# Kernel tuning notes

Measured on AMD Instinct MI355X. Metric: run time of the kernel, lower is better.

## Reference

```python
import jax, jax.numpy as jnp
import numpy as np

_PROFILE = [2, 3, 4]  # direction exponents per scale -> 4, 8, 16 directions


def _make_filter_banks():
    """Build per-scale grouped-conv filter banks.
    Returns list of arrays [3*num_dirs, 1, k, k] (same filters tiled for R,G,B groups)."""
    banks = []
    for scale, exp in enumerate(_PROFILE):
        num_dirs = 2 ** exp
        size = 11 + 4 * scale
        center = size // 2
        coords = np.arange(size) - center
        X, Y = np.meshgrid(coords, coords)
        kernels = []
        for d in range(num_dirs):
            angle = np.pi * d / num_dirs
            Xr = X * np.cos(angle) + Y * np.sin(angle)
            Yr = -X * np.sin(angle) + Y * np.cos(angle)
            freq = 0.3 / 2 ** scale
            dir_bandwidth = 2.0
            env = np.exp(-(Xr ** 2 + (dir_bandwidth * Yr) ** 2) / (2 * (size / 4) ** 2))
            k = env * np.cos(2 * np.pi * freq * Xr)
            k = k / (np.abs(k).sum() + 1e-8)
            kernels.append(k)
        bank = np.stack(kernels)[:, None]          # [nd, 1, k, k]
        bank = np.tile(bank, (3, 1, 1, 1))          # [3*nd, 1, k, k] (groups = RGB)
        banks.append(jnp.asarray(bank, dtype=jnp.float32))
    return banks


def setup_inputs() -> dict:
    key = jax.random.key(0)
    rgb_image = jax.random.normal(key, (4, 3, 512, 512), dtype=jnp.float32)
    f0, f1, f2 = _make_filter_banks()
    return {"rgb_image": rgb_image, "f0": f0, "f1": f1, "f2": f2}


def _grouped_conv(x, w):
    # x: [B,3,H,W], w: [3*nd,1,k,k]; SAME padding (k odd), one group per RGB channel.
    p = w.shape[-1] // 2
    return jax.lax.conv_general_dilated(
        x, w, window_strides=(1, 1), padding=[(p, p), (p, p)],
        feature_group_count=3,
        dimension_numbers=("NCHW", "OIHW", "NCHW"))


def reference(rgb_image, f0, f1, f2):
    B, C, H, W = rgb_image.shape
    # Directional subbands per scale, grouped by channel: [B, 3, nd, H, W]
    s0 = _grouped_conv(rgb_image, f0).reshape(B, 3, 4, H, W)
    s1 = _grouped_conv(rgb_image, f1).reshape(B, 3, 8, H, W)
    s2 = _grouped_conv(rgb_image, f2).reshape(B, 3, 16, H, W)
    # Low-frequency branch: avg_pool2d(k=4,s=4) then bilinear upsample (align_corners=False)
    low = rgb_image.reshape(B, 3, H // 4, 4, W // 4, 4).mean(axis=(3, 5))
    low = jax.image.resize(low, (B, 3, H, W), method="linear")
    low = low[:, :, None]  # [B, 3, 1, H, W]
    # Per channel: [s0 dirs, s1 dirs, s2 dirs, low] -> 29 bands; 3 channels -> 87
    out = jnp.concatenate([s0, s1, s2, low], axis=2).reshape(B, 87, H, W)
    return out
```

## Files before the change

kernel.cpp:

```cpp
#include <hip/hip_runtime.h>
#include <hip/hip_bf16.h>

#define HW 512

typedef __attribute__((ext_vector_type(8))) short bf16x8;
typedef __attribute__((ext_vector_type(16))) float floatx16;

union BFrag { uint2 u2[2]; bf16x8 v; };

static __device__ inline ushort f2bf(float f) {
    __hip_bfloat16 h = __float2bfloat16(f);
    return *(ushort*)&h;
}

__device__ __align__(16) short g_afrag[(18 + 27 + 30) * 256 * 8];

template<int K, int NDIR, int SUB0, int OCTS, int NSTEP, int AOFF>
__device__ __forceinline__
void conv_body(ushort* __restrict__ s_img,
               const float* __restrict__ img, float* __restrict__ out,
               const int plane)
{
    constexpr int YPACK   = 32 / NDIR;
    constexpr int R       = K / 2;
    constexpr int TILE_W  = 128, TILE_H = 32;
    constexpr int NCHAIN  = TILE_H / YPACK;
    constexpr int CB      = 4;
    constexpr int NPASS   = NCHAIN / CB;
    constexpr int ROWS_A  = K + YPACK - 1;
    constexpr int EXT_Y   = (TILE_H - YPACK) + ROWS_A;
    constexpr int EXT_X   = 4 * 31 + 8 * (OCTS - 1) + 8;
    constexpr int SPX     = (EXT_X + 7) & ~7;
    constexpr int P       = (OCTS == 3) ? 3 : 1;
    constexpr int GSTRIDE = (2 * P / OCTS) * SPX;
    constexpr int NG      = NSTEP / P;
    static_assert(NSTEP % P == 0, "octet chunking must be exact");
    static_assert(NSTEP * 2 == ROWS_A * OCTS, "step count must cover octets");

    const int tid   = threadIdx.x;
    const int bx    = blockIdx.x, by = blockIdx.y;
    const int bb    = plane / 3, cc = plane % 3;
    const float* __restrict__ src = img + (size_t)plane * HW * HW;
    const int gx0 = bx * TILE_W, gy0 = by * TILE_H;

    constexpr int PAIRS = SPX / 2;
    for (int idx = tid; idx < EXT_Y * PAIRS; idx += 256) {
        const int row = idx / PAIRS;
        const int col = (idx - row * PAIRS) * 2;
        const int gy = gy0 - R + row;
        const int gx = gx0 - R + col;
        float v0 = 0.f, v1 = 0.f;
        if ((unsigned)gy < HW) {
            if ((unsigned)gx       < HW) v0 = src[gy * HW + gx];
            if ((unsigned)(gx + 1) < HW) v1 = src[gy * HW + gx + 1];
        }
        *(uint*)&s_img[row * SPX + col] = ((uint)f2bf(v1) << 16) | (uint)f2bf(v0);
    }
    __syncthreads();

    const int lane = tid & 63;
    const int r    = tid >> 6;
    const int n    = lane & 31;
    const int h    = lane >> 5;

    int base0[P];
    #pragma unroll
    for (int s0 = 0; s0 < P; ++s0) {
        const int c0   = 2 * s0 + h;
        const int dyu0 = c0 / OCTS, o0 = c0 - dyu0 * OCTS;
        base0[s0] = dyu0 * SPX + 8 * o0 + 4 * n;
    }

    const int px = gx0 + r + 4 * n;
    const short* __restrict__ abase = g_afrag + ((size_t)AOFF + tid) * 8;

    for (int p = 0; p < NPASS; ++p) {
        floatx16 acc[CB] = {};
        const ushort* bp = s_img + p * (CB * YPACK * SPX);
        const short*  ap = abase;
        for (int gi = 0; gi < NG; ++gi) {
            #pragma unroll
            for (int s0 = 0; s0 < P; ++s0) {
                const bf16x8 a = *(const bf16x8*)(ap + s0 * 256 * 8);
                #pragma unroll
                for (int i = 0; i < CB; ++i) {
                    const ushort* q = bp + (base0[s0] + i * (YPACK * SPX));
                    BFrag b;
                    b.u2[0] = *(const uint2*)q;
                    b.u2[1] = *(const uint2*)(q + 4);
                    acc[i] = __builtin_amdgcn_mfma_f32_32x32x16_bf16(a, b.v, acc[i], 0, 0, 0);
                }
            }
            bp += GSTRIDE;
            ap += P * 256 * 8;
        }
        #pragma unroll
        for (int i = 0; i < CB; ++i) {
            #pragma unroll
            for (int reg = 0; reg < 16; ++reg) {
                const int m  = (reg & 3) + 8 * (reg >> 2) + 4 * h;
                const int dd = m & (NDIR - 1);
                const int yo = m / NDIR;
                const int Y  = gy0 + (p * CB + i) * YPACK + yo;
                out[((size_t)(bb * 87 + cc * 29 + SUB0 + dd) * HW + Y) * HW + px] = acc[i][reg];
            }
        }
    }
}

#define SMEM_ELEMS 7600

__global__ __launch_bounds__(256, 4)
void fused_conv(const float* __restrict__ img, float* __restrict__ out)
{
    __shared__ __align__(16) ushort s_img[SMEM_ELEMS];
    const int z  = blockIdx.z;
    const int sc = z % 3;
    const int plane = z / 3;
    if (sc == 0) {
        conv_body<19, 16, 12, 3, 30, (18 + 27) * 256>(s_img, img, out, plane);
    } else if (sc == 1) {
        conv_body<15,  8,  4, 3, 27, 18 * 256>(s_img, img, out, plane);
    } else {
        conv_body<11,  4,  0, 2, 18, 0>(s_img, img, out, plane);
    }
}

template<int K, int NDIR, int OCTS, int NSTEP, int AOFF>
__device__ __forceinline__
void prep_body(const float* __restrict__ filt)
{
    const int tid  = threadIdx.x;
    const int lane = tid & 63, r = tid >> 6;
    const int m    = lane & 31, h = lane >> 5;
    const int dirm  = m & (NDIR - 1);
    const int yoffm = m / NDIR;
    for (int s = 0; s < NSTEP; ++s) {
        bf16x8 v;
        #pragma unroll
        for (int j = 0; j < 8; ++j) {
            const int c   = 2 * s + h;
            const int dyu = c / OCTS, o = c - dyu * OCTS;
            const int dy  = dyu - yoffm;
            const int dx  = 8 * o + j - r;
            float fv = 0.f;
            if (dy >= 0 && dy < K && dx >= 0 && dx < K)
                fv = filt[(dirm * K + dy) * K + dx];
            v[j] = (short)f2bf(fv);
        }
        *(bf16x8*)&g_afrag[((size_t)AOFF + s * 256 + tid) * 8] = v;
    }
}

__global__ __launch_bounds__(256)
void prep_afrag(const float* __restrict__ f0, const float* __restrict__ f1,
                const float* __restrict__ f2)
{
    if (blockIdx.x == 0)      prep_body<11,  4, 2, 18, 0>(f0);
    else if (blockIdx.x == 1) prep_body<15,  8, 3, 27, 18 * 256>(f1);
    else                      prep_body<19, 16, 3, 30, (18 + 27) * 256>(f2);
}

__global__ __launch_bounds__(256)
void low_kernel(const float* __restrict__ img, float* __restrict__ out)
{
    __shared__ float s_p[34 * 35];
    const int tid   = threadIdx.x;
    const int bx    = blockIdx.x, by = blockIdx.y;
    const int plane = blockIdx.z;
    const int b     = plane / 3, c = plane % 3;
    const float* __restrict__ src = img + (size_t)plane * HW * HW;
    const int lx0 = bx * 32, ly0 = by * 32;

    for (int idx = tid; idx < 34 * 34; idx += 256) {
        const int r = idx / 34, col = idx % 34;
        const int ly = min(max(ly0 - 1 + r,   0), 127);
        const int lx = min(max(lx0 - 1 + col, 0), 127);
        const float* p = src + (size_t)(ly * 4) * HW + lx * 4;
        float s = 0.f;
        #pragma unroll
        for (int rr = 0; rr < 4; ++rr) {
            const float4 v = *(const float4*)(p + (size_t)rr * HW);
            s += v.x + v.y + v.z + v.w;
        }
        s_p[r * 35 + col] = s * (1.f / 16.f);
    }
    __syncthreads();

    const size_t outbase = (size_t)(b * 87 + c * 29 + 28) * HW * HW;
    for (int k = 0; k < 64; ++k) {
        const int pix = tid + k * 256;
        const int ry = pix >> 7, rx = pix & 127;
        const int gy = ly0 * 4 + ry, gx = lx0 * 4 + rx;
        const float cy = (gy - 1.5f) * 0.25f;
        const float cx = (gx - 1.5f) * 0.25f;
        const int jy = (int)floorf(cy), jx = (int)floorf(cx);
        const float fy = cy - jy, fx = cx - jx;
        const int tyy = jy - (ly0 - 1);
        const int txx = jx - (lx0 - 1);
        const float p00 = s_p[tyy * 35 + txx],       p01 = s_p[tyy * 35 + txx + 1];
        const float p10 = s_p[(tyy + 1) * 35 + txx], p11 = s_p[(tyy + 1) * 35 + txx + 1];
        const float v0 = p00 + fx * (p01 - p00);
        const float v1 = p10 + fx * (p11 - p10);
        out[outbase + (size_t)gy * HW + gx] = v0 + fy * (v1 - v0);
    }
}

extern "C" void kernel_launch(void* const* d_in, const int* in_sizes, int n_in,
                              void* d_out, int out_size, void* d_ws, size_t ws_size,
                              hipStream_t stream)
{
    const float* img = (const float*)d_in[0];
    const float* f0  = (const float*)d_in[1];
    const float* f1  = (const float*)d_in[2];
    const float* f2  = (const float*)d_in[3];
    float* out = (float*)d_out;

    dim3 block(256);
    prep_afrag<<<dim3(3), block, 0, stream>>>(f0, f1, f2);
    fused_conv<<<dim3(HW / 128, HW / 32, 36), block, 0, stream>>>(img, out);
    low_kernel<<<dim3(4, 4, 12), block, 0, stream>>>(img, out);
}
```

Baseline: 563.0 us.

## Switch conv MFMA from 32x32x16 to 16x16x32 with narrower tiles

Replaces the 32x32x16 bf16 MFMA with 16x16x32, halving the rows packed per MFMA (YPACK) and doubling the K depth per step, which reduces the number of zero-padded Toeplitz steps per filter. Tiles shrink to 64 wide, shared memory drops, launch bounds allow 8 blocks per CU, and the grid doubles in x. Filter fragment prep is spread over 34 blocks, one step each. The aim is less wasted MFMA work on padded filter taps and higher occupancy, at the cost of more halo reloads and more loop unrolling.

```diff
diff --git a/kernel.cpp b/kernel.cpp
--- a/kernel.cpp
+++ b/kernel.cpp
@@ -4,7 +4,7 @@
 #define HW 512
 
 typedef __attribute__((ext_vector_type(8))) short bf16x8;
-typedef __attribute__((ext_vector_type(16))) float floatx16;
+typedef __attribute__((ext_vector_type(4))) float floatx4;
 
 union BFrag { uint2 u2[2]; bf16x8 v; };
 
@@ -13,7 +13,7 @@
     return *(ushort*)&h;
 }
 
-__device__ __align__(16) short g_afrag[(18 + 27 + 30) * 256 * 8];
+__device__ __align__(16) short g_afrag[(7 + 12 + 15) * 256 * 8];
 
 template<int K, int NDIR, int SUB0, int OCTS, int NSTEP, int AOFF>
 __device__ __forceinline__
@@ -21,21 +21,21 @@
                const float* __restrict__ img, float* __restrict__ out,
                const int plane)
 {
-    constexpr int YPACK   = 32 / NDIR;
+    constexpr int YPACK   = 16 / NDIR;
     constexpr int R       = K / 2;
-    constexpr int TILE_W  = 128, TILE_H = 32;
+    constexpr int TILE_W  = 64, TILE_H = 32;
     constexpr int NCHAIN  = TILE_H / YPACK;
     constexpr int CB      = 4;
     constexpr int NPASS   = NCHAIN / CB;
-    constexpr int ROWS_A  = K + YPACK - 1;
-    constexpr int EXT_Y   = (TILE_H - YPACK) + ROWS_A;
-    constexpr int EXT_X   = 4 * 31 + 8 * (OCTS - 1) + 8;
+    constexpr int ROWSP   = (4 * NSTEP - 1) / OCTS + 1;
+    constexpr int EXT_Y   = (TILE_H - YPACK) + ROWSP;
+    constexpr int EXT_X   = 4 * 15 + 8 * (OCTS - 1) + 8;
     constexpr int SPX     = (EXT_X + 7) & ~7;
     constexpr int P       = (OCTS == 3) ? 3 : 1;
-    constexpr int GSTRIDE = (2 * P / OCTS) * SPX;
+    constexpr int GSTRIDE = (4 * P / OCTS) * SPX;
     constexpr int NG      = NSTEP / P;
-    static_assert(NSTEP % P == 0, "octet chunking must be exact");
-    static_assert(NSTEP * 2 == ROWS_A * OCTS, "step count must cover octets");
+    static_assert(NSTEP % P == 0, "");
+    static_assert(NCHAIN % CB == 0, "");
 
     const int tid   = threadIdx.x;
     const int bx    = blockIdx.x, by = blockIdx.y;
@@ -60,47 +60,46 @@
 
     const int lane = tid & 63;
     const int r    = tid >> 6;
-    const int n    = lane & 31;
-    const int h    = lane >> 5;
+    const int mn   = lane & 15;
+    const int q    = lane >> 4;
 
     int base0[P];
     #pragma unroll
     for (int s0 = 0; s0 < P; ++s0) {
-        const int c0   = 2 * s0 + h;
+        const int c0   = 4 * s0 + q;
         const int dyu0 = c0 / OCTS, o0 = c0 - dyu0 * OCTS;
-        base0[s0] = dyu0 * SPX + 8 * o0 + 4 * n;
-    }
-
-    const int px = gx0 + r + 4 * n;
+        base0[s0] = dyu0 * SPX + 8 * o0 + 4 * mn;
+    }
+
+    const int px = gx0 + r + 4 * mn;
     const short* __restrict__ abase = g_afrag + ((size_t)AOFF + tid) * 8;
 
     for (int p = 0; p < NPASS; ++p) {
-        floatx16 acc[CB] = {};
+        floatx4 acc[CB] = {};
         const ushort* bp = s_img + p * (CB * YPACK * SPX);
-        const short*  ap = abase;
-        for (int gi = 0; gi < NG; ++gi) {
+        #pragma unroll
+        for (int g = 0; g < NG; ++g) {
             #pragma unroll
             for (int s0 = 0; s0 < P; ++s0) {
-                const bf16x8 a = *(const bf16x8*)(ap + s0 * 256 * 8);
+                const int s = g * P + s0;
+                const bf16x8 a = *(const bf16x8*)(abase + s * 2048);
                 #pragma unroll
                 for (int i = 0; i < CB; ++i) {
-                    const ushort* q = bp + (base0[s0] + i * (YPACK * SPX));
+                    const ushort* qp = bp + (base0[s0] + g * GSTRIDE + i * (YPACK * SPX));
                     BFrag b;
-                    b.u2[0] = *(const uint2*)q;
-                    b.u2[1] = *(const uint2*)(q + 4);
-                    acc[i] = __builtin_amdgcn_mfma_f32_32x32x16_bf16(a, b.v, acc[i], 0, 0, 0);
+                    b.u2[0] = *(const uint2*)qp;
+                    b.u2[1] = *(const uint2*)(qp + 4);
+                    acc[i] = __builtin_amdgcn_mfma_f32_16x16x32_bf16(a, b.v, acc[i], 0, 0, 0);
                 }
             }
-            bp += GSTRIDE;
-            ap += P * 256 * 8;
         }
         #pragma unroll
         for (int i = 0; i < CB; ++i) {
             #pragma unroll
-            for (int reg = 0; reg < 16; ++reg) {
-                const int m  = (reg & 3) + 8 * (reg >> 2) + 4 * h;
-                const int dd = m & (NDIR - 1);
-                const int yo = m / NDIR;
+            for (int reg = 0; reg < 4; ++reg) {
+                const int mrow = q * 4 + reg;
+                const int dd = mrow & (NDIR - 1);
+                const int yo = mrow / NDIR;
                 const int Y  = gy0 + (p * CB + i) * YPACK + yo;
                 out[((size_t)(bb * 87 + cc * 29 + SUB0 + dd) * HW + Y) * HW + px] = acc[i][reg];
             }
@@ -108,9 +107,9 @@
     }
 }
 
-#define SMEM_ELEMS 7600
-
-__global__ __launch_bounds__(256, 4)
+#define SMEM_ELEMS 4488
+
+__global__ __launch_bounds__(256, 8)
 void fused_conv(const float* __restrict__ img, float* __restrict__ out)
 {
     __shared__ __align__(16) ushort s_img[SMEM_ELEMS];
@@ -118,47 +117,46 @@
     const int sc = z % 3;
     const int plane = z / 3;
     if (sc == 0) {
-        conv_body<19, 16, 12, 3, 30, (18 + 27) * 256>(s_img, img, out, plane);
+        conv_body<19, 16, 12, 3, 15, (7 + 12) * 256>(s_img, img, out, plane);
     } else if (sc == 1) {
-        conv_body<15,  8,  4, 3, 27, 18 * 256>(s_img, img, out, plane);
+        conv_body<15,  8,  4, 3, 12, 7 * 256>(s_img, img, out, plane);
     } else {
-        conv_body<11,  4,  0, 2, 18, 0>(s_img, img, out, plane);
-    }
-}
-
-template<int K, int NDIR, int OCTS, int NSTEP, int AOFF>
+        conv_body<11,  4,  0, 2,  7, 0>(s_img, img, out, plane);
+    }
+}
+
+template<int K, int NDIR, int OCTS, int AOFF>
 __device__ __forceinline__
-void prep_body(const float* __restrict__ filt)
+void prep_step(const float* __restrict__ filt, const int s)
 {
     const int tid  = threadIdx.x;
     const int lane = tid & 63, r = tid >> 6;
-    const int m    = lane & 31, h = lane >> 5;
-    const int dirm  = m & (NDIR - 1);
-    const int yoffm = m / NDIR;
-    for (int s = 0; s < NSTEP; ++s) {
-        bf16x8 v;
-        #pragma unroll
-        for (int j = 0; j < 8; ++j) {
-            const int c   = 2 * s + h;
-            const int dyu = c / OCTS, o = c - dyu * OCTS;
-            const int dy  = dyu - yoffm;
-            const int dx  = 8 * o + j - r;
-            float fv = 0.f;
-            if (dy >= 0 && dy < K && dx >= 0 && dx < K)
-                fv = filt[(dirm * K + dy) * K + dx];
-            v[j] = (short)f2bf(fv);
-        }
-        *(bf16x8*)&g_afrag[((size_t)AOFF + s * 256 + tid) * 8] = v;
-    }
+    const int mn   = lane & 15, q = lane >> 4;
+    const int dirm  = mn & (NDIR - 1);
+    const int yoffm = mn / NDIR;
+    bf16x8 v;
+    #pragma unroll
+    for (int j = 0; j < 8; ++j) {
+        const int c   = 4 * s + q;
+        const int dyu = c / OCTS, o = c - dyu * OCTS;
+        const int dy  = dyu - yoffm;
+        const int dx  = 8 * o + j - r;
+        float fv = 0.f;
+        if (dy >= 0 && dy < K && dx >= 0 && dx < K)
+            fv = filt[(dirm * K + dy) * K + dx];
+        v[j] = (short)f2bf(fv);
+    }
+    *(bf16x8*)&g_afrag[((size_t)AOFF + s * 256 + tid) * 8] = v;
 }
 
 __global__ __launch_bounds__(256)
 void prep_afrag(const float* __restrict__ f0, const float* __restrict__ f1,
                 const float* __restrict__ f2)
 {
-    if (blockIdx.x == 0)      prep_body<11,  4, 2, 18, 0>(f0);
-    else if (blockIdx.x == 1) prep_body<15,  8, 3, 27, 18 * 256>(f1);
-    else                      prep_body<19, 16, 3, 30, (18 + 27) * 256>(f2);
+    const int sb = blockIdx.x;
+    if (sb < 7)       prep_step<11,  4, 2, 0>(f0, sb);
+    else if (sb < 19) prep_step<15,  8, 3, 7 * 256>(f1, sb - 7);
+    else              prep_step<19, 16, 3, (7 + 12) * 256>(f2, sb - 19);
 }
 
 __global__ __launch_bounds__(256)
@@ -217,7 +215,7 @@
     float* out = (float*)d_out;
 
     dim3 block(256);
-    prep_afrag<<<dim3(3), block, 0, stream>>>(f0, f1, f2);
-    fused_conv<<<dim3(HW / 128, HW / 32, 36), block, 0, stream>>>(img, out);
+    prep_afrag<<<dim3(34), block, 0, stream>>>(f0, f1, f2);
+    fused_conv<<<dim3(HW / 64, HW / 32, 36), block, 0, stream>>>(img, out);
     low_kernel<<<dim3(4, 4, 12), block, 0, stream>>>(img, out);
 }
```

Result: slower. 592.2 us (+5.2%).
